# Optimization experiments

Measured on AMD Instinct MI355X. Metric: run time of the kernel, lower is better.

Reference implementation:

```python
import jax, jax.numpy as jnp
import numpy as np

G, N_PER_G, V, H, DIN, DOUT, E = 1024, 64, 32, 128, 128, 10, 1048576
N = G * N_PER_G


def _lin(key, fan_in, fan_out):
    k1, k2 = jax.random.split(key)
    s = 1.0 / np.sqrt(fan_in)
    return (jax.random.uniform(k1, (fan_in, fan_out), jnp.float32, -s, s),
            jax.random.uniform(k2, (fan_out,), jnp.float32, -s, s))


def setup_inputs() -> dict:
    key = jax.random.key(0)
    ks = jax.random.split(key, 16)
    x = jax.random.normal(ks[0], (N, DIN), jnp.float32)
    # random edges constrained within each graph's contiguous node block
    gid = jax.random.randint(ks[1], (E,), 0, G)
    src = gid * N_PER_G + jax.random.randint(ks[2], (E,), 0, N_PER_G)
    dst = gid * N_PER_G + jax.random.randint(ks[3], (E,), 0, N_PER_G)
    edge_index = jnp.stack([src, dst]).astype(jnp.int64)
    batch = jnp.repeat(jnp.arange(G, dtype=jnp.int64), N_PER_G)
    edge_weights = jnp.ones((G, N_PER_G, V), jnp.float32) / V  # uniform init
    vemb = jax.random.normal(ks[4], (G, V, H), jnp.float32)
    vemb = vemb / jnp.linalg.norm(vemb, axis=-1, keepdims=True)
    W_emb, b_emb = _lin(ks[5], DIN, H)
    W_gcn, b_gcn = _lin(ks[6], H, H)
    aff_W1, aff_b1 = _lin(ks[7], H, H)
    aff_W2, aff_b2 = _lin(ks[8], H, H)
    vn_W1, vn_b1 = _lin(ks[9], H, H)
    vn_W2, vn_b2 = _lin(ks[10], H, H)
    mlp_W1, mlp_b1 = _lin(ks[11], H, H)
    mlp_W2, mlp_b2 = _lin(ks[12], H, DOUT)
    return dict(x=x, edge_index=edge_index, batch=batch, edge_weights=edge_weights,
                vemb=vemb, W_emb=W_emb, b_emb=b_emb, W_gcn=W_gcn, b_gcn=b_gcn,
                aff_W1=aff_W1, aff_b1=aff_b1, aff_W2=aff_W2, aff_b2=aff_b2,
                vn_W1=vn_W1, vn_b1=vn_b1, vn_W2=vn_W2, vn_b2=vn_b2,
                mlp_W1=mlp_W1, mlp_b1=mlp_b1, mlp_W2=mlp_W2, mlp_b2=mlp_b2)


def reference(x, edge_index, batch, edge_weights, vemb, W_emb, b_emb, W_gcn, b_gcn,
              aff_W1, aff_b1, aff_W2, aff_b2, vn_W1, vn_b1, vn_W2, vn_b2,
              mlp_W1, mlp_b1, mlp_W2, mlp_b2):
    n_nodes = x.shape[0]
    g, n, v = edge_weights.shape
    h = x @ W_emb + b_emb                                   # node embedding
    # GCNConv with self-loops and symmetric normalization
    hw = h @ W_gcn
    sl = jnp.arange(n_nodes)
    s = jnp.concatenate([edge_index[0], sl])
    d = jnp.concatenate([edge_index[1], sl])
    deg = jax.ops.segment_sum(jnp.ones_like(d, dtype=h.dtype), d, num_segments=n_nodes)
    inv = jax.lax.rsqrt(jnp.maximum(deg, 1.0))
    msg = hw[s] * (inv[s] * inv[d])[:, None]                # [E+N, H]
    h = jax.nn.relu(jax.ops.segment_sum(msg, d, num_segments=n_nodes) + b_gcn)
    # affinity MLP
    aff = jax.nn.relu(h @ aff_W1 + aff_b1) @ aff_W2 + aff_b2
    hg = h.reshape(g, n, -1)
    affg = aff.reshape(g, n, -1)
    # attention vs fixed normalized virtual-node embeddings
    att = jnp.einsum('gnh,gvh->gnv', affg, vemb) / jnp.sqrt(jnp.asarray(hg.shape[-1], h.dtype))
    ew = edge_weights * (1.0 + jax.nn.sigmoid(att))
    rs = ew.sum(axis=-1, keepdims=True)
    ew = ew / jnp.where(rs == 0, 1.0, rs)                   # row-normalize
    vn = jnp.einsum('gnv,gnh->gvh', ew, hg)                 # weighted scatter-pool
    vn = jax.nn.relu(vn @ vn_W1 + vn_b1) @ vn_W2 + vn_b2
    gf = vn.mean(axis=1)                                    # [G, H]
    return jax.nn.relu(gf @ mlp_W1 + mlp_b1) @ mlp_W2 + mlp_b2
```

## Files before the change

kernel.cpp:

```cpp
#include <hip/hip_runtime.h>
#include <hip/hip_bf16.h>
#include <cstddef>


#define EDGES 1048576
#define CAP 2048
#define SR 136
#define ST 72

typedef __attribute__((ext_vector_type(8))) short short8;
typedef __attribute__((ext_vector_type(4))) float f32x4;
typedef __hip_bfloat16 bf;
struct __align__(8) bf4 { bf v[4]; };

__global__ __launch_bounds__(256) void edge_hist(const int* __restrict__ ei,
                                                 unsigned* __restrict__ H)
{
    __shared__ unsigned lh[1024];
    int tid = threadIdx.x, b = blockIdx.x;
    for (int t = tid; t < 1024; t += 256) lh[t] = 0;
    __syncthreads();
    int base = b * 4096;
#pragma unroll 4
    for (int t = 0; t < 16; ++t) {
        int s = ei[base + t * 256 + tid];
        atomicAdd(&lh[s >> 6], 1u);
    }
    __syncthreads();
    for (int t = tid; t < 1024; t += 256) H[b * 1024 + t] = lh[t];
}

__global__ __launch_bounds__(256) void scan_conv(
    unsigned* __restrict__ H, unsigned* __restrict__ Tot,
    const float* __restrict__ w0, const float* __restrict__ w1,
    const float* __restrict__ w2, const float* __restrict__ w3,
    const float* __restrict__ w4, const float* __restrict__ w5,
    bf* __restrict__ outw)
{
    int b = blockIdx.x;
    if (b < 256) {
        int wv = threadIdx.x >> 6, lane = threadIdx.x & 63;
        int g = b * 4 + wv;
        unsigned v[4];
#pragma unroll
        for (int c = 0; c < 4; ++c) v[c] = H[(c * 64 + lane) * 1024 + g];
        unsigned run = 0;
#pragma unroll
        for (int c = 0; c < 4; ++c) {
            unsigned s = v[c];
            unsigned incl = s;
#pragma unroll
            for (int d = 1; d < 64; d <<= 1) {
                unsigned t = __shfl_up(incl, d);
                if (lane >= d) incl += t;
            }
            H[(c * 64 + lane) * 1024 + g] = run + (incl - s);
            run += __shfl(incl, 63);
        }
        if (lane == 0) Tot[g] = run;
    } else {
        int idx = (b - 256) * 256 + threadIdx.x;
        int n = idx >> 7, k = idx & 127;
        int off = (((n >> 4) * 4 + (k >> 5)) * 512) + (n & 15) * 32 + (k & 31);
        const float* srcs[6] = { w0, w1, w2, w3, w4, w5 };
#pragma unroll
        for (int m = 0; m < 6; ++m) {
            float vv = (m == 3) ? srcs[m][n * 128 + k] : srcs[m][k * 128 + n];
            outw[m * 16384 + off] = __float2bfloat16(vv);
        }
    }
}

__global__ __launch_bounds__(256) void edge_scatter(const int* __restrict__ ei,
                                                    const unsigned* __restrict__ H,
                                                    unsigned short* __restrict__ sorted)
{
    __shared__ unsigned lh[1024];
    __shared__ unsigned hrow[1024];
    int tid = threadIdx.x, b = blockIdx.x;
    for (int t = tid; t < 1024; t += 256) { lh[t] = 0; hrow[t] = H[b * 1024 + t]; }
    __syncthreads();
    int base = b * 4096;
    for (int t = 0; t < 16; ++t) {
        int e = base + t * 256 + tid;
        int s = ei[e], d = ei[EDGES + e];
        int g = s >> 6;
        unsigned r = atomicAdd(&lh[g], 1u);
        unsigned o = hrow[g] + r;
        if (o < (unsigned)CAP)
            sorted[(unsigned)g * CAP + o] = (unsigned short)(((d & 63) << 6) | (s & 63));
    }
}

__device__ __forceinline__ void loadB(const bf* __restrict__ gW, int wv, int l15,
                                      int kofs, short8* B)
{
#pragma unroll
    for (int ks = 0; ks < 4; ++ks)
        B[ks] = *(const short8*)(gW + (wv * 4 + ks) * 512 + l15 * 32 + kofs);
}

template<int MT, int KS, int SA>
__device__ __forceinline__ void mmaAB(const bf* sA, int rowA, int l15, int kofs,
                                      const short8* B, f32x4* acc)
{
#pragma unroll
    for (int ks = 0; ks < KS; ++ks) {
        short8 a[MT];
#pragma unroll
        for (int m = 0; m < MT; ++m)
            a[m] = *(const short8*)(sA + (rowA + m * 16 + l15) * SA + ks * 32 + kofs);
#pragma unroll
        for (int m = 0; m < MT; ++m)
            acc[m] = __builtin_amdgcn_mfma_f32_16x16x32_bf16(a[m], B[ks], acc[m], 0, 0, 0);
    }
}

template<int NT, int KS, int SB>
__device__ __forceinline__ void mmaBA(const bf* sB, int rowB, int l15, int kofs,
                                      const short8* A, f32x4* acc)
{
#pragma unroll
    for (int ks = 0; ks < KS; ++ks) {
        short8 b[NT];
#pragma unroll
        for (int nt = 0; nt < NT; ++nt)
            b[nt] = *(const short8*)(sB + (rowB + nt * 16 + l15) * SB + ks * 32 + kofs);
#pragma unroll
        for (int nt = 0; nt < NT; ++nt)
            acc[nt] = __builtin_amdgcn_mfma_f32_16x16x32_bf16(A[ks], b[nt], acc[nt], 0, 0, 0);
    }
}

template<int MT, int KS, int SA, int SB>
__device__ __forceinline__ void mmaABlds(const bf* sA, int rowA, const bf* sB, int rowB,
                                         int l15, int kofs, f32x4* acc)
{
#pragma unroll
    for (int ks = 0; ks < KS; ++ks) {
        short8 bb = *(const short8*)(sB + (rowB + l15) * SB + ks * 32 + kofs);
        short8 a[MT];
#pragma unroll
        for (int m = 0; m < MT; ++m)
            a[m] = *(const short8*)(sA + (rowA + m * 16 + l15) * SA + ks * 32 + kofs);
#pragma unroll
        for (int m = 0; m < MT; ++m)
            acc[m] = __builtin_amdgcn_mfma_f32_16x16x32_bf16(a[m], bb, acc[m], 0, 0, 0);
    }
}

__global__ __launch_bounds__(512, 2) void fused_graph(
    const float* __restrict__ x, const float* __restrict__ edge_w,
    const float* __restrict__ vemb, const bf* __restrict__ gWb,
    const float* __restrict__ b_emb,  const float* __restrict__ b_gcn,
    const float* __restrict__ aff_b1, const float* __restrict__ aff_b2,
    const float* __restrict__ vn_b1,  const float* __restrict__ vn_b2,
    const float* __restrict__ mlp_W1, const float* __restrict__ mlp_b1,
    const float* __restrict__ mlp_W2, const float* __restrict__ mlp_b2,
    const unsigned short* __restrict__ sorted,
    const unsigned* __restrict__ Tot,
    float* __restrict__ out)
{
    __shared__ __align__(16) bf sRM1[64 * SR];
    __shared__ __align__(16) bf sRM2[64 * SR];
    __shared__ __align__(16) bf sT1 [128 * ST];
    __shared__ __align__(16) bf sT2 [128 * ST];
    __shared__ __align__(16) bf sAdj[64 * ST];
    __shared__ float sInv[64];
    __shared__ float sBatt[32];

    unsigned* cnt = (unsigned*)sT1;
    bf* sVemb = sAdj;
    float* sPart = (float*)(sAdj + 4352);
    bf* sS    = sT1;
    bf* sEwnT = sT1 + 4608;
    float* sT2f = (float*)sT2;

    const int tid = threadIdx.x;
    const int g = blockIdx.x;
    const int wv = tid >> 6;
    const int lane = tid & 63;
    const int l15 = lane & 15;
    const int q = lane >> 4;
    const int kofs = q * 8;
    const int c = wv * 16 + l15;
    const int fq = wv * 16 + q * 4;

    short8 Bp[4], Bn[4];
    loadB(gWb, wv, l15, kofs, Bp);
    loadB(gWb + 16384, wv, l15, kofs, Bn);
    float4 xreg[4];
    const float4* gx = (const float4*)(x + (size_t)g * 8192);
#pragma unroll
    for (int t = 0; t < 4; ++t) xreg[t] = gx[tid + t * 512];
    float4 vreg[2];
    const float4* gv = (const float4*)(vemb + (size_t)g * 4096);
#pragma unroll
    for (int t = 0; t < 2; ++t) vreg[t] = gv[tid + t * 512];
    const int p6row = (wv & 3) * 16;
    const int p6v   = (wv >> 2) * 16 + l15;
    float ewreg[4];
#pragma unroll
    for (int r = 0; r < 4; ++r)
        ewreg[r] = edge_w[(size_t)g * 2048 + (p6row + q * 4 + r) * 32 + p6v];
    float bias_g = b_gcn[c];
    unsigned ecnt = min(Tot[g], (unsigned)CAP);
    unsigned ebase = (unsigned)g * CAP;

#pragma unroll
    for (int t = 0; t < 2; ++t) cnt[tid * 2 + t] = 0u;
    __syncthreads();
    for (unsigned i = tid; i < ecnt; i += 512) {
        unsigned w = sorted[ebase + i];
        unsigned d = w >> 6, s = w & 63u;
        atomicAdd(&cnt[d * 16 + (s >> 2)], 1u << ((s & 3u) * 8));
    }
#pragma unroll
    for (int t = 0; t < 4; ++t) {
        int i = tid + t * 512;
        int row = i >> 5, c4 = i & 31;
        float4 w = xreg[t];
        bf4 tt;
        tt.v[0] = __float2bfloat16(w.x); tt.v[1] = __float2bfloat16(w.y);
        tt.v[2] = __float2bfloat16(w.z); tt.v[3] = __float2bfloat16(w.w);
        *(bf4*)(sRM1 + row * SR + c4 * 4) = tt;
    }
    __syncthreads();

    {
        int r = tid >> 3, q8 = tid & 7;
        float rs = 0.f;
#pragma unroll
        for (int t = 0; t < 2; ++t) {
            unsigned wd = cnt[r * 16 + q8 * 2 + t];
#pragma unroll
            for (int j = 0; j < 4; ++j) {
                int s = (q8 * 2 + t) * 4 + j;
                float v = (float)((wd >> (j * 8)) & 255u) + (s == r ? 1.f : 0.f);
                rs += v;
                sAdj[r * ST + s] = __float2bfloat16(v);
            }
        }
        rs += __shfl_xor(rs, 1);
        rs += __shfl_xor(rs, 2);
        rs += __shfl_xor(rs, 4);
        if (q8 == 0) sInv[r] = rsqrtf(rs);
    }
    {
        f32x4 acc[4] = {};
        mmaBA<4, 4, SR>(sRM1, 0, l15, kofs, Bp, acc);
        loadB(gWb + 2 * 16384, wv, l15, kofs, Bp);
        f32x4 b4 = *(const f32x4*)(b_emb + fq);
#pragma unroll
        for (int nt = 0; nt < 4; ++nt) {
            bf4 tv;
#pragma unroll
            for (int r = 0; r < 4; ++r) tv.v[r] = __float2bfloat16(acc[nt][r] + b4[r]);
            *(bf4*)(sRM2 + (nt * 16 + l15) * SR + fq) = tv;
        }
    }
    __syncthreads();

    {
        f32x4 acc[4] = {};
        mmaAB<4, 4, SR>(sRM2, 0, l15, kofs, Bn, acc);
        loadB(gWb + 3 * 16384, wv, l15, kofs, Bn);
#pragma unroll
        for (int m = 0; m < 4; ++m) {
            bf4 tv;
#pragma unroll
            for (int r = 0; r < 4; ++r)
                tv.v[r] = __float2bfloat16(acc[m][r] * sInv[m * 16 + q * 4 + r]);
            *(bf4*)(sT1 + c * ST + m * 16 + q * 4) = tv;
        }
    }
    __syncthreads();

    {
        f32x4 acc[4] = {};
        mmaABlds<4, 2, ST, ST>(sAdj, 0, sT1, wv * 16, l15, kofs, acc);
#pragma unroll
        for (int m = 0; m < 4; ++m) {
            bf4 tv;
#pragma unroll
            for (int r = 0; r < 4; ++r) {
                float v = fmaxf(acc[m][r] * sInv[m * 16 + q * 4 + r] + bias_g, 0.f);
                sRM1[(m * 16 + q * 4 + r) * SR + c] = __float2bfloat16(v);
                tv.v[r] = __float2bfloat16(v);
            }
            *(bf4*)(sT2 + c * ST + m * 16 + q * 4) = tv;
        }
    }
    __syncthreads();

    {
#pragma unroll
        for (int t = 0; t < 2; ++t) {
            int i = tid + t * 512;
            int v = i >> 5, o4 = i & 31;
            float4 w = vreg[t];
            bf4 tt;
            tt.v[0] = __float2bfloat16(w.x); tt.v[1] = __float2bfloat16(w.y);
            tt.v[2] = __float2bfloat16(w.z); tt.v[3] = __float2bfloat16(w.w);
            *(bf4*)(sVemb + v * SR + o4 * 4) = tt;
        }
        f32x4 acc[4] = {};
        mmaBA<4, 4, SR>(sRM1, 0, l15, kofs, Bp, acc);
        loadB(gWb + 4 * 16384, wv, l15, kofs, Bp);
        f32x4 b4 = *(const f32x4*)(aff_b1 + fq);
#pragma unroll
        for (int nt = 0; nt < 4; ++nt) {
            bf4 tv;
#pragma unroll
            for (int r = 0; r < 4; ++r)
                tv.v[r] = __float2bfloat16(fmaxf(acc[nt][r] + b4[r], 0.f));
            *(bf4*)(sRM2 + (nt * 16 + l15) * SR + fq) = tv;
        }
    }
    __syncthreads();

    {
        f32x4 acc[2] = {};
        mmaBA<2, 4, SR>(sVemb, 0, l15, kofs, Bn, acc);
        loadB(gWb + 5 * 16384, wv, l15, kofs, Bn);
#pragma unroll
        for (int nt = 0; nt < 2; ++nt) {
            bf4 tv;
#pragma unroll
            for (int r = 0; r < 4; ++r) tv.v[r] = __float2bfloat16(acc[nt][r]);
            *(bf4*)(sS + (nt * 16 + l15) * SR + fq) = tv;
        }
        if (tid < 256) {
            int v = tid >> 3, sg = tid & 7;
            float s = 0.f;
            const bf* pv = sVemb + v * SR + sg * 16;
            const float* pb = aff_b2 + sg * 16;
#pragma unroll
            for (int o = 0; o < 16; ++o) s += pb[o] * __bfloat162float(pv[o]);
            s += __shfl_xor(s, 1); s += __shfl_xor(s, 2); s += __shfl_xor(s, 4);
            if (sg == 0) sBatt[v] = s;
        }
    }
    __syncthreads();

    {
        f32x4 acc = {};
        const int hv = wv >> 2;
#pragma unroll
        for (int ks = 0; ks < 4; ++ks) {
            short8 bb = *(const short8*)(sS + (hv * 16 + l15) * SR + ks * 32 + kofs);
            short8 a  = *(const short8*)(sRM2 + (p6row + l15) * SR + ks * 32 + kofs);
            acc = __builtin_amdgcn_mfma_f32_16x16x32_bf16(a, bb, acc, 0, 0, 0);
        }
        const float sc = 0.08838834764831845f;
        float bt = sBatt[p6v];
        float e[4];
#pragma unroll
        for (int r = 0; r < 4; ++r) {
            float att = (acc[r] + bt) * sc;
            e[r] = ewreg[r] * (1.f + 1.f / (1.f + __expf(-att)));
            float rs = e[r];
            rs += __shfl_xor(rs, 1); rs += __shfl_xor(rs, 2);
            rs += __shfl_xor(rs, 4); rs += __shfl_xor(rs, 8);
            if (l15 == 0) sPart[hv * 64 + p6row + q * 4 + r] = rs;
        }
        __syncthreads();
        bf4 tv;
#pragma unroll
        for (int r = 0; r < 4; ++r) {
            float rs = sPart[p6row + q * 4 + r] + sPart[64 + p6row + q * 4 + r];
            tv.v[r] = __float2bfloat16(e[r] / rs);
        }
        *(bf4*)(sEwnT + (hv * 16 + l15) * ST + p6row + q * 4) = tv;
    }
    __syncthreads();

    {
        f32x4 acc[2] = {};
#pragma unroll
        for (int ks = 0; ks < 2; ++ks) {
            short8 af = *(const short8*)(sT2 + (wv * 16 + l15) * ST + ks * 32 + kofs);
            short8 b0 = *(const short8*)(sEwnT + l15 * ST + ks * 32 + kofs);
            short8 b1 = *(const short8*)(sEwnT + (16 + l15) * ST + ks * 32 + kofs);
            acc[0] = __builtin_amdgcn_mfma_f32_16x16x32_bf16(af, b0, acc[0], 0, 0, 0);
            acc[1] = __builtin_amdgcn_mfma_f32_16x16x32_bf16(af, b1, acc[1], 0, 0, 0);
        }
#pragma unroll
        for (int nt = 0; nt < 2; ++nt) {
            bf4 tv;
#pragma unroll
            for (int r = 0; r < 4; ++r) tv.v[r] = __float2bfloat16(acc[nt][r]);
            *(bf4*)(sRM1 + (nt * 16 + l15) * SR + fq) = tv;
        }
    }
    __syncthreads();

    {
        f32x4 acc[2] = {};
        mmaBA<2, 4, SR>(sRM1, 0, l15, kofs, Bp, acc);
        f32x4 b4 = *(const f32x4*)(vn_b1 + fq);
#pragma unroll
        for (int nt = 0; nt < 2; ++nt) {
            bf4 tv;
#pragma unroll
            for (int r = 0; r < 4; ++r)
                tv.v[r] = __float2bfloat16(fmaxf(acc[nt][r] + b4[r], 0.f));
            *(bf4*)(sRM1 + (32 + nt * 16 + l15) * SR + fq) = tv;
        }
    }
    __syncthreads();

    {
        float bias_v2 = vn_b2[c];
        f32x4 acc[2] = {};
        mmaAB<2, 4, SR>(sRM1 + 32 * SR, 0, l15, kofs, Bn, acc);
#pragma unroll
        for (int m = 0; m < 2; ++m)
#pragma unroll
            for (int r = 0; r < 4; ++r)
                sT2f[c * 34 + m * 16 + q * 4 + r] = acc[m][r] + bias_v2;
    }
    __syncthreads();

    float* sF = (float*)sRM2;
    if (tid < 128) {
        float s = 0.f;
#pragma unroll
        for (int v = 0; v < 32; ++v) s += sT2f[tid * 34 + v];
        sF[tid] = s * 0.03125f;
    }
    __syncthreads();

    {
        int o = tid & 127, hh = tid >> 7;
        const float* w = mlp_W1 + (size_t)(hh * 32) * 128 + o;
        float a = 0.f;
#pragma unroll 8
        for (int k = 0; k < 32; ++k) a = fmaf(sF[hh * 32 + k], w[k * 128], a);
        sF[128 + hh * 128 + o] = a;
    }
    __syncthreads();
    if (tid < 128)
        sF[640 + tid] = fmaxf(sF[128 + tid] + sF[256 + tid] + sF[384 + tid]
                              + sF[512 + tid] + mlp_b1[tid], 0.f);
    __syncthreads();

    if (tid < 80) {
        int oo = tid >> 3, jg = tid & 7;
        float p = 0.f;
#pragma unroll
        for (int t2 = 0; t2 < 16; ++t2) {
            int j = jg * 16 + t2;
            p = fmaf(sF[640 + j], mlp_W2[j * 10 + oo], p);
        }
        p += __shfl_xor(p, 1); p += __shfl_xor(p, 2); p += __shfl_xor(p, 4);
        if (jg == 0) out[g * 10 + oo] = p + mlp_b2[oo];
    }
}

extern "C" void kernel_launch(void* const* d_in, const int* in_sizes, int n_in,
                              void* d_out, int out_size, void* d_ws, size_t ws_size,
                              hipStream_t stream)
{
    const float* x       = (const float*)d_in[0];
    const int*   ei      = (const int*)  d_in[1];
    const float* edge_w  = (const float*)d_in[3];
    const float* vemb    = (const float*)d_in[4];
    const float* W_emb   = (const float*)d_in[5];
    const float* b_emb   = (const float*)d_in[6];
    const float* W_gcn   = (const float*)d_in[7];
    const float* b_gcn   = (const float*)d_in[8];
    const float* aff_W1  = (const float*)d_in[9];
    const float* aff_b1  = (const float*)d_in[10];
    const float* aff_W2  = (const float*)d_in[11];
    const float* aff_b2  = (const float*)d_in[12];
    const float* vn_W1   = (const float*)d_in[13];
    const float* vn_b1   = (const float*)d_in[14];
    const float* vn_W2   = (const float*)d_in[15];
    const float* vn_b2   = (const float*)d_in[16];
    const float* mlp_W1  = (const float*)d_in[17];
    const float* mlp_b1  = (const float*)d_in[18];
    const float* mlp_W2  = (const float*)d_in[19];
    const float* mlp_b2  = (const float*)d_in[20];

    char* ws = (char*)d_ws;
    unsigned short* sorted = (unsigned short*)ws;
    unsigned* H    = (unsigned*)(ws + (4u << 20));
    unsigned* Tot  = (unsigned*)(ws + (5u << 20));
    bf*       gWb  = (bf*)      (ws + (5u << 20) + 65536);

    edge_hist  <<<dim3(256), dim3(256), 0, stream>>>(ei, H);
    scan_conv  <<<dim3(320), dim3(256), 0, stream>>>(
        H, Tot, W_emb, W_gcn, aff_W1, aff_W2, vn_W1, vn_W2, gWb);
    edge_scatter<<<dim3(256),dim3(256), 0, stream>>>(ei, H, sorted);
    fused_graph<<<dim3(1024), dim3(512), 0, stream>>>(
        x, edge_w, vemb, gWb, b_emb, b_gcn, aff_b1, aff_b2,
        vn_b1, vn_b2, mlp_W1, mlp_b1, mlp_W2, mlp_b2,
        sorted, Tot, (float*)d_out);
}
```

Baseline: 181.9 us.

## Process two graphs per block to amortize weight fragment loads and barriers

Each block now handles two graphs instead of one, so the grid is halved. Shared buffers are doubled, and every stage loops over both graphs before a shared barrier. The intent is to reuse each register-resident weight B fragment across two graphs, halving global weight-fragment loads and barriers per graph. The cost is double the LDS and more registers per block, and launch bounds drop to one block per SM, which reduces occupancy and latency hiding.

```diff
diff --git a/kernel.cpp b/kernel.cpp
--- a/kernel.cpp
+++ b/kernel.cpp
@@ -149,7 +149,7 @@
     }
 }
 
-__global__ __launch_bounds__(512, 2) void fused_graph(
+__global__ __launch_bounds__(512, 1) void fused_graph(
     const float* __restrict__ x, const float* __restrict__ edge_w,
     const float* __restrict__ vemb, const bf* __restrict__ gWb,
     const float* __restrict__ b_emb,  const float* __restrict__ b_gcn,
@@ -161,23 +161,16 @@
     const unsigned* __restrict__ Tot,
     float* __restrict__ out)
 {
-    __shared__ __align__(16) bf sRM1[64 * SR];
-    __shared__ __align__(16) bf sRM2[64 * SR];
-    __shared__ __align__(16) bf sT1 [128 * ST];
-    __shared__ __align__(16) bf sT2 [128 * ST];
-    __shared__ __align__(16) bf sAdj[64 * ST];
-    __shared__ float sInv[64];
-    __shared__ float sBatt[32];
-
-    unsigned* cnt = (unsigned*)sT1;
-    bf* sVemb = sAdj;
-    float* sPart = (float*)(sAdj + 4352);
-    bf* sS    = sT1;
-    bf* sEwnT = sT1 + 4608;
-    float* sT2f = (float*)sT2;
+    __shared__ __align__(16) bf sRM1[2 * 64 * SR];
+    __shared__ __align__(16) bf sRM2[2 * 64 * SR];
+    __shared__ __align__(16) bf sT1 [2 * 128 * ST];
+    __shared__ __align__(16) bf sT2 [2 * 128 * ST];
+    __shared__ __align__(16) bf sAdj[2 * 64 * ST];
+    __shared__ float sInv[2 * 64];
+    __shared__ float sBatt[2 * 32];
 
     const int tid = threadIdx.x;
-    const int g = blockIdx.x;
+    const int g0 = blockIdx.x * 2;
     const int wv = tid >> 6;
     const int lane = tid & 63;
     const int l15 = lane & 15;
@@ -185,128 +178,164 @@
     const int kofs = q * 8;
     const int c = wv * 16 + l15;
     const int fq = wv * 16 + q * 4;
+    const int p6row = (wv & 3) * 16;
+    const int hv = wv >> 2;
+    const int p6v = hv * 16 + l15;
 
     short8 Bp[4], Bn[4];
     loadB(gWb, wv, l15, kofs, Bp);
     loadB(gWb + 16384, wv, l15, kofs, Bn);
-    float4 xreg[4];
-    const float4* gx = (const float4*)(x + (size_t)g * 8192);
-#pragma unroll
-    for (int t = 0; t < 4; ++t) xreg[t] = gx[tid + t * 512];
-    float4 vreg[2];
-    const float4* gv = (const float4*)(vemb + (size_t)g * 4096);
-#pragma unroll
-    for (int t = 0; t < 2; ++t) vreg[t] = gv[tid + t * 512];
-    const int p6row = (wv & 3) * 16;
-    const int p6v   = (wv >> 2) * 16 + l15;
-    float ewreg[4];
-#pragma unroll
-    for (int r = 0; r < 4; ++r)
-        ewreg[r] = edge_w[(size_t)g * 2048 + (p6row + q * 4 + r) * 32 + p6v];
+    float4 xreg[2][4];
+    float4 vreg[2][2];
+    float ewreg[2][4];
+    unsigned ecnt[2], ebase[2];
+#pragma unroll
+    for (int gg = 0; gg < 2; ++gg) {
+        const float4* gx = (const float4*)(x + (size_t)(g0 + gg) * 8192);
+#pragma unroll
+        for (int t = 0; t < 4; ++t) xreg[gg][t] = gx[tid + t * 512];
+        const float4* gv = (const float4*)(vemb + (size_t)(g0 + gg) * 4096);
+#pragma unroll
+        for (int t = 0; t < 2; ++t) vreg[gg][t] = gv[tid + t * 512];
+#pragma unroll
+        for (int r = 0; r < 4; ++r)
+            ewreg[gg][r] = edge_w[(size_t)(g0 + gg) * 2048
+                                  + (p6row + q * 4 + r) * 32 + p6v];
+        ecnt[gg] = min(Tot[g0 + gg], (unsigned)CAP);
+        ebase[gg] = (unsigned)(g0 + gg) * CAP;
+    }
     float bias_g = b_gcn[c];
-    unsigned ecnt = min(Tot[g], (unsigned)CAP);
-    unsigned ebase = (unsigned)g * CAP;
-
-#pragma unroll
-    for (int t = 0; t < 2; ++t) cnt[tid * 2 + t] = 0u;
-    __syncthreads();
-    for (unsigned i = tid; i < ecnt; i += 512) {
-        unsigned w = sorted[ebase + i];
-        unsigned d = w >> 6, s = w & 63u;
-        atomicAdd(&cnt[d * 16 + (s >> 2)], 1u << ((s & 3u) * 8));
-    }
-#pragma unroll
-    for (int t = 0; t < 4; ++t) {
-        int i = tid + t * 512;
-        int row = i >> 5, c4 = i & 31;
-        float4 w = xreg[t];
-        bf4 tt;
-        tt.v[0] = __float2bfloat16(w.x); tt.v[1] = __float2bfloat16(w.y);
-        tt.v[2] = __float2bfloat16(w.z); tt.v[3] = __float2bfloat16(w.w);
-        *(bf4*)(sRM1 + row * SR + c4 * 4) = tt;
-    }
-    __syncthreads();
-
-    {
-        int r = tid >> 3, q8 = tid & 7;
-        float rs = 0.f;
-#pragma unroll
-        for (int t = 0; t < 2; ++t) {
-            unsigned wd = cnt[r * 16 + q8 * 2 + t];
-#pragma unroll
-            for (int j = 0; j < 4; ++j) {
-                int s = (q8 * 2 + t) * 4 + j;
-                float v = (float)((wd >> (j * 8)) & 255u) + (s == r ? 1.f : 0.f);
-                rs += v;
-                sAdj[r * ST + s] = __float2bfloat16(v);
+
+#pragma unroll
+    for (int gg = 0; gg < 2; ++gg) {
+        unsigned* cntg = (unsigned*)(sT1 + gg * 128 * ST);
+#pragma unroll
+        for (int t = 0; t < 2; ++t) cntg[tid * 2 + t] = 0u;
+    }
+    __syncthreads();
+#pragma unroll
+    for (int gg = 0; gg < 2; ++gg) {
+        unsigned* cntg = (unsigned*)(sT1 + gg * 128 * ST);
+        bf* RM1g = sRM1 + gg * 64 * SR;
+        for (unsigned i = tid; i < ecnt[gg]; i += 512) {
+            unsigned w = sorted[ebase[gg] + i];
+            unsigned d = w >> 6, s = w & 63u;
+            atomicAdd(&cntg[d * 16 + (s >> 2)], 1u << ((s & 3u) * 8));
+        }
+#pragma unroll
+        for (int t = 0; t < 4; ++t) {
+            int i = tid + t * 512;
+            int row = i >> 5, c4 = i & 31;
+            float4 w = xreg[gg][t];
+            bf4 tt;
+            tt.v[0] = __float2bfloat16(w.x); tt.v[1] = __float2bfloat16(w.y);
+            tt.v[2] = __float2bfloat16(w.z); tt.v[3] = __float2bfloat16(w.w);
+            *(bf4*)(RM1g + row * SR + c4 * 4) = tt;
+        }
+    }
+    __syncthreads();
+
+#pragma unroll
+    for (int gg = 0; gg < 2; ++gg) {
+        unsigned* cntg = (unsigned*)(sT1 + gg * 128 * ST);
+        bf* Adjg = sAdj + gg * 64 * ST;
+        float* Invg = sInv + gg * 64;
+        {
+            int r = tid >> 3, q8 = tid & 7;
+            float rs = 0.f;
+#pragma unroll
+            for (int t = 0; t < 2; ++t) {
+                unsigned wd = cntg[r * 16 + q8 * 2 + t];
+#pragma unroll
+                for (int j = 0; j < 4; ++j) {
+                    int s = (q8 * 2 + t) * 4 + j;
+                    float v = (float)((wd >> (j * 8)) & 255u) + (s == r ? 1.f : 0.f);
+                    rs += v;
+                    Adjg[r * ST + s] = __float2bfloat16(v);
+                }
             }
-        }
-        rs += __shfl_xor(rs, 1);
-        rs += __shfl_xor(rs, 2);
-        rs += __shfl_xor(rs, 4);
-        if (q8 == 0) sInv[r] = rsqrtf(rs);
-    }
-    {
+            rs += __shfl_xor(rs, 1);
+            rs += __shfl_xor(rs, 2);
+            rs += __shfl_xor(rs, 4);
+            if (q8 == 0) Invg[r] = rsqrtf(rs);
+        }
+        bf* RM1g = sRM1 + gg * 64 * SR;
+        bf* RM2g = sRM2 + gg * 64 * SR;
+        {
+            f32x4 acc[4] = {};
+            mmaBA<4, 4, SR>(RM1g, 0, l15, kofs, Bp, acc);
+            f32x4 b4 = *(const f32x4*)(b_emb + fq);
+#pragma unroll
+            for (int nt = 0; nt < 4; ++nt) {
+                bf4 tv;
+#pragma unroll
+                for (int r = 0; r < 4; ++r) tv.v[r] = __float2bfloat16(acc[nt][r] + b4[r]);
+                *(bf4*)(RM2g + (nt * 16 + l15) * SR + fq) = tv;
+            }
+        }
+    }
+    loadB(gWb + 2 * 16384, wv, l15, kofs, Bp);
+    __syncthreads();
+
+#pragma unroll
+    for (int gg = 0; gg < 2; ++gg) {
+        bf* RM2g = sRM2 + gg * 64 * SR;
+        bf* T1g = sT1 + gg * 128 * ST;
+        float* Invg = sInv + gg * 64;
         f32x4 acc[4] = {};
-        mmaBA<4, 4, SR>(sRM1, 0, l15, kofs, Bp, acc);
-        loadB(gWb + 2 * 16384, wv, l15, kofs, Bp);
-        f32x4 b4 = *(const f32x4*)(b_emb + fq);
-#pragma unroll
-        for (int nt = 0; nt < 4; ++nt) {
-            bf4 tv;
-#pragma unroll
-            for (int r = 0; r < 4; ++r) tv.v[r] = __float2bfloat16(acc[nt][r] + b4[r]);
-            *(bf4*)(sRM2 + (nt * 16 + l15) * SR + fq) = tv;
-        }
-    }
-    __syncthreads();
-
-    {
-        f32x4 acc[4] = {};
-        mmaAB<4, 4, SR>(sRM2, 0, l15, kofs, Bn, acc);
-        loadB(gWb + 3 * 16384, wv, l15, kofs, Bn);
+        mmaAB<4, 4, SR>(RM2g, 0, l15, kofs, Bn, acc);
 #pragma unroll
         for (int m = 0; m < 4; ++m) {
             bf4 tv;
 #pragma unroll
             for (int r = 0; r < 4; ++r)
-                tv.v[r] = __float2bfloat16(acc[m][r] * sInv[m * 16 + q * 4 + r]);
-            *(bf4*)(sT1 + c * ST + m * 16 + q * 4) = tv;
-        }
-    }
-    __syncthreads();
-
-    {
+                tv.v[r] = __float2bfloat16(acc[m][r] * Invg[m * 16 + q * 4 + r]);
+            *(bf4*)(T1g + c * ST + m * 16 + q * 4) = tv;
+        }
+    }
+    loadB(gWb + 3 * 16384, wv, l15, kofs, Bn);
+    __syncthreads();
+
+#pragma unroll
+    for (int gg = 0; gg < 2; ++gg) {
+        bf* Adjg = sAdj + gg * 64 * ST;
+        bf* T1g = sT1 + gg * 128 * ST;
+        bf* RM1g = sRM1 + gg * 64 * SR;
+        bf* T2g = sT2 + gg * 128 * ST;
+        float* Invg = sInv + gg * 64;
         f32x4 acc[4] = {};
-        mmaABlds<4, 2, ST, ST>(sAdj, 0, sT1, wv * 16, l15, kofs, acc);
+        mmaABlds<4, 2, ST, ST>(Adjg, 0, T1g, wv * 16, l15, kofs, acc);
 #pragma unroll
         for (int m = 0; m < 4; ++m) {
             bf4 tv;
 #pragma unroll
             for (int r = 0; r < 4; ++r) {
-                float v = fmaxf(acc[m][r] * sInv[m * 16 + q * 4 + r] + bias_g, 0.f);
-                sRM1[(m * 16 + q * 4 + r) * SR + c] = __float2bfloat16(v);
+                float v = fmaxf(acc[m][r] * Invg[m * 16 + q * 4 + r] + bias_g, 0.f);
+                RM1g[(m * 16 + q * 4 + r) * SR + c] = __float2bfloat16(v);
                 tv.v[r] = __float2bfloat16(v);
             }
-            *(bf4*)(sT2 + c * ST + m * 16 + q * 4) = tv;
-        }
-    }
-    __syncthreads();
-
-    {
+            *(bf4*)(T2g + c * ST + m * 16 + q * 4) = tv;
+        }
+    }
+    __syncthreads();
+
+#pragma unroll
+    for (int gg = 0; gg < 2; ++gg) {
+        bf* Vembg = sAdj + gg * 64 * ST;
 #pragma unroll
         for (int t = 0; t < 2; ++t) {
             int i = tid + t * 512;
             int v = i >> 5, o4 = i & 31;
-            float4 w = vreg[t];
+            float4 w = vreg[gg][t];
             bf4 tt;
             tt.v[0] = __float2bfloat16(w.x); tt.v[1] = __float2bfloat16(w.y);
             tt.v[2] = __float2bfloat16(w.z); tt.v[3] = __float2bfloat16(w.w);
-            *(bf4*)(sVemb + v * SR + o4 * 4) = tt;
-        }
+            *(bf4*)(Vembg + v * SR + o4 * 4) = tt;
+        }
+        bf* RM1g = sRM1 + gg * 64 * SR;
+        bf* RM2g = sRM2 + gg * 64 * SR;
         f32x4 acc[4] = {};
-        mmaBA<4, 4, SR>(sRM1, 0, l15, kofs, Bp, acc);
-        loadB(gWb + 4 * 16384, wv, l15, kofs, Bp);
+        mmaBA<4, 4, SR>(RM1g, 0, l15, kofs, Bp, acc);
         f32x4 b4 = *(const f32x4*)(aff_b1 + fq);
 #pragma unroll
         for (int nt = 0; nt < 4; ++nt) {
@@ -314,74 +343,92 @@
 #pragma unroll
             for (int r = 0; r < 4; ++r)
                 tv.v[r] = __float2bfloat16(fmaxf(acc[nt][r] + b4[r], 0.f));
-            *(bf4*)(sRM2 + (nt * 16 + l15) * SR + fq) = tv;
-        }
-    }
-    __syncthreads();
-
-    {
+            *(bf4*)(RM2g + (nt * 16 + l15) * SR + fq) = tv;
+        }
+    }
+    loadB(gWb + 4 * 16384, wv, l15, kofs, Bp);
+    __syncthreads();
+
+#pragma unroll
+    for (int gg = 0; gg < 2; ++gg) {
+        bf* Vembg = sAdj + gg * 64 * ST;
+        bf* Sg = sT1 + gg * 128 * ST;
+        float* Battg = sBatt + gg * 32;
         f32x4 acc[2] = {};
-        mmaBA<2, 4, SR>(sVemb, 0, l15, kofs, Bn, acc);
-        loadB(gWb + 5 * 16384, wv, l15, kofs, Bn);
+        mmaBA<2, 4, SR>(Vembg, 0, l15, kofs, Bn, acc);
 #pragma unroll
         for (int nt = 0; nt < 2; ++nt) {
             bf4 tv;
 #pragma unroll
             for (int r = 0; r < 4; ++r) tv.v[r] = __float2bfloat16(acc[nt][r]);
-            *(bf4*)(sS + (nt * 16 + l15) * SR + fq) = tv;
+            *(bf4*)(Sg + (nt * 16 + l15) * SR + fq) = tv;
         }
         if (tid < 256) {
             int v = tid >> 3, sg = tid & 7;
             float s = 0.f;
-            const bf* pv = sVemb + v * SR + sg * 16;
+            const bf* pv = Vembg + v * SR + sg * 16;
             const float* pb = aff_b2 + sg * 16;
 #pragma unroll
             for (int o = 0; o < 16; ++o) s += pb[o] * __bfloat162float(pv[o]);
             s += __shfl_xor(s, 1); s += __shfl_xor(s, 2); s += __shfl_xor(s, 4);
-            if (sg == 0) sBatt[v] = s;
-        }
-    }
-    __syncthreads();
-
-    {
+            if (sg == 0) Battg[v] = s;
+        }
+    }
+    loadB(gWb + 5 * 16384, wv, l15, kofs, Bn);
+    __syncthreads();
+
+    float e2[2][4];
+#pragma unroll
+    for (int gg = 0; gg < 2; ++gg) {
+        bf* RM2g = sRM2 + gg * 64 * SR;
+        bf* Sg = sT1 + gg * 128 * ST;
+        float* Battg = sBatt + gg * 32;
+        float* Partg = (float*)(sAdj + gg * 64 * ST + 4352);
         f32x4 acc = {};
-        const int hv = wv >> 2;
 #pragma unroll
         for (int ks = 0; ks < 4; ++ks) {
-            short8 bb = *(const short8*)(sS + (hv * 16 + l15) * SR + ks * 32 + kofs);
-            short8 a  = *(const short8*)(sRM2 + (p6row + l15) * SR + ks * 32 + kofs);
+            short8 bb = *(const short8*)(Sg + (hv * 16 + l15) * SR + ks * 32 + kofs);
+            short8 a  = *(const short8*)(RM2g + (p6row + l15) * SR + ks * 32 + kofs);
             acc = __builtin_amdgcn_mfma_f32_16x16x32_bf16(a, bb, acc, 0, 0, 0);
         }
         const float sc = 0.08838834764831845f;
-        float bt = sBatt[p6v];
-        float e[4];
+        float bt = Battg[p6v];
 #pragma unroll
         for (int r = 0; r < 4; ++r) {
             float att = (acc[r] + bt) * sc;
-            e[r] = ewreg[r] * (1.f + 1.f / (1.f + __expf(-att)));
-            float rs = e[r];
+            e2[gg][r] = ewreg[gg][r] * (1.f + 1.f / (1.f + __expf(-att)));
+            float rs = e2[gg][r];
             rs += __shfl_xor(rs, 1); rs += __shfl_xor(rs, 2);
             rs += __shfl_xor(rs, 4); rs += __shfl_xor(rs, 8);
-            if (l15 == 0) sPart[hv * 64 + p6row + q * 4 + r] = rs;
-        }
-        __syncthreads();
+            if (l15 == 0) Partg[hv * 64 + p6row + q * 4 + r] = rs;
+        }
+    }
+    __syncthreads();
+#pragma unroll
+    for (int gg = 0; gg < 2; ++gg) {
+        float* Partg = (float*)(sAdj + gg * 64 * ST + 4352);
+        bf* EwnTg = sT1 + gg * 128 * ST + 4608;
         bf4 tv;
 #pragma unroll
         for (int r = 0; r < 4; ++r) {
-            float rs = sPart[p6row + q * 4 + r] + sPart[64 + p6row + q * 4 + r];
-            tv.v[r] = __float2bfloat16(e[r] / rs);
-        }
-        *(bf4*)(sEwnT + (hv * 16 + l15) * ST + p6row + q * 4) = tv;
-    }
-    __syncthreads();
-
-    {
+            float rs = Partg[p6row + q * 4 + r] + Partg[64 + p6row + q * 4 + r];
+            tv.v[r] = __float2bfloat16(e2[gg][r] / rs);
+        }
+        *(bf4*)(EwnTg + (hv * 16 + l15) * ST + p6row + q * 4) = tv;
+    }
+    __syncthreads();
+
+#pragma unroll
+    for (int gg = 0; gg < 2; ++gg) {
+        bf* T2g = sT2 + gg * 128 * ST;
+        bf* EwnTg = sT1 + gg * 128 * ST + 4608;
+        bf* RM1g = sRM1 + gg * 64 * SR;
         f32x4 acc[2] = {};
 #pragma unroll
         for (int ks = 0; ks < 2; ++ks) {
-            short8 af = *(const short8*)(sT2 + (wv * 16 + l15) * ST + ks * 32 + kofs);
-            short8 b0 = *(const short8*)(sEwnT + l15 * ST + ks * 32 + kofs);
-            short8 b1 = *(const short8*)(sEwnT + (16 + l15) * ST + ks * 32 + kofs);
+            short8 af = *(const short8*)(T2g + (wv * 16 + l15) * ST + ks * 32 + kofs);
+            short8 b0 = *(const short8*)(EwnTg + l15 * ST + ks * 32 + kofs);
+            short8 b1 = *(const short8*)(EwnTg + (16 + l15) * ST + ks * 32 + kofs);
             acc[0] = __builtin_amdgcn_mfma_f32_16x16x32_bf16(af, b0, acc[0], 0, 0, 0);
             acc[1] = __builtin_amdgcn_mfma_f32_16x16x32_bf16(af, b1, acc[1], 0, 0, 0);
         }
@@ -390,14 +437,16 @@
             bf4 tv;
 #pragma unroll
             for (int r = 0; r < 4; ++r) tv.v[r] = __float2bfloat16(acc[nt][r]);
-            *(bf4*)(sRM1 + (nt * 16 + l15) * SR + fq) = tv;
-        }
-    }
-    __syncthreads();
-
-    {
+            *(bf4*)(RM1g + (nt * 16 + l15) * SR + fq) = tv;
+        }
+    }
+    __syncthreads();
+
+#pragma unroll
+    for (int gg = 0; gg < 2; ++gg) {
+        bf* RM1g = sRM1 + gg * 64 * SR;
         f32x4 acc[2] = {};
-        mmaBA<2, 4, SR>(sRM1, 0, l15, kofs, Bp, acc);
+        mmaBA<2, 4, SR>(RM1g, 0, l15, kofs, Bp, acc);
         f32x4 b4 = *(const f32x4*)(vn_b1 + fq);
 #pragma unroll
         for (int nt = 0; nt < 2; ++nt) {
@@ -405,56 +454,75 @@
 #pragma unroll
             for (int r = 0; r < 4; ++r)
                 tv.v[r] = __float2bfloat16(fmaxf(acc[nt][r] + b4[r], 0.f));
-            *(bf4*)(sRM1 + (32 + nt * 16 + l15) * SR + fq) = tv;
+            *(bf4*)(RM1g + (32 + nt * 16 + l15) * SR + fq) = tv;
         }
     }
     __syncthreads();
 
     {
         float bias_v2 = vn_b2[c];
-        f32x4 acc[2] = {};
-        mmaAB<2, 4, SR>(sRM1 + 32 * SR, 0, l15, kofs, Bn, acc);
-#pragma unroll
-        for (int m = 0; m < 2; ++m)
-#pragma unroll
-            for (int r = 0; r < 4; ++r)
-                sT2f[c * 34 + m * 16 + q * 4 + r] = acc[m][r] + bias_v2;
-    }
-    __syncthreads();
-
-    float* sF = (float*)sRM2;
-    if (tid < 128) {
-        float s = 0.f;
-#pragma unroll
-        for (int v = 0; v < 32; ++v) s += sT2f[tid * 34 + v];
-        sF[tid] = s * 0.03125f;
-    }
-    __syncthreads();
-
-    {
+#pragma unroll
+        for (int gg = 0; gg < 2; ++gg) {
+            bf* RM1g = sRM1 + gg * 64 * SR;
+            float* T2fg = (float*)(sT2 + gg * 128 * ST);
+            f32x4 acc[2] = {};
+            mmaAB<2, 4, SR>(RM1g + 32 * SR, 0, l15, kofs, Bn, acc);
+#pragma unroll
+            for (int m = 0; m < 2; ++m)
+#pragma unroll
+                for (int r = 0; r < 4; ++r)
+                    T2fg[c * 34 + m * 16 + q * 4 + r] = acc[m][r] + bias_v2;
+        }
+    }
+    __syncthreads();
+
+#pragma unroll
+    for (int gg = 0; gg < 2; ++gg) {
+        float* T2fg = (float*)(sT2 + gg * 128 * ST);
+        float* sFg = (float*)(sRM2 + gg * 64 * SR);
+        if (tid < 128) {
+            float s = 0.f;
+#pragma unroll
+            for (int v = 0; v < 32; ++v) s += T2fg[tid * 34 + v];
+            sFg[tid] = s * 0.03125f;
+        }
+    }
+    __syncthreads();
+
+#pragma unroll
+    for (int gg = 0; gg < 2; ++gg) {
+        float* sFg = (float*)(sRM2 + gg * 64 * SR);
         int o = tid & 127, hh = tid >> 7;
         const float* w = mlp_W1 + (size_t)(hh * 32) * 128 + o;
         float a = 0.f;
 #pragma unroll 8
-        for (int k = 0; k < 32; ++k) a = fmaf(sF[hh * 32 + k], w[k * 128], a);
-        sF[128 + hh * 128 + o] = a;
-    }
-    __syncthreads();
-    if (tid < 128)
-        sF[640 + tid] = fmaxf(sF[128 + tid] + sF[256 + tid] + sF[384 + tid]
-                              + sF[512 + tid] + mlp_b1[tid], 0.f);
-    __syncthreads();
-
-    if (tid < 80) {
-        int oo = tid >> 3, jg = tid & 7;
-        float p = 0.f;
-#pragma unroll
-        for (int t2 = 0; t2 < 16; ++t2) {
-            int j = jg * 16 + t2;
-            p = fmaf(sF[640 + j], mlp_W2[j * 10 + oo], p);
-        }
-        p += __shfl_xor(p, 1); p += __shfl_xor(p, 2); p += __shfl_xor(p, 4);
-        if (jg == 0) out[g * 10 + oo] = p + mlp_b2[oo];
+        for (int k = 0; k < 32; ++k) a = fmaf(sFg[hh * 32 + k], w[k * 128], a);
+        sFg[128 + hh * 128 + o] = a;
+    }
+    __syncthreads();
+#pragma unroll
+    for (int gg = 0; gg < 2; ++gg) {
+        float* sFg = (float*)(sRM2 + gg * 64 * SR);
+        if (tid < 128)
+            sFg[640 + tid] = fmaxf(sFg[128 + tid] + sFg[256 + tid] + sFg[384 + tid]
+                                   + sFg[512 + tid] + mlp_b1[tid], 0.f);
+    }
+    __syncthreads();
+
+#pragma unroll
+    for (int gg = 0; gg < 2; ++gg) {
+        float* sFg = (float*)(sRM2 + gg * 64 * SR);
+        if (tid < 80) {
+            int oo = tid >> 3, jg = tid & 7;
+            float p = 0.f;
+#pragma unroll
+            for (int t2 = 0; t2 < 16; ++t2) {
+                int j = jg * 16 + t2;
+                p = fmaf(sFg[640 + j], mlp_W2[j * 10 + oo], p);
+            }
+            p += __shfl_xor(p, 1); p += __shfl_xor(p, 2); p += __shfl_xor(p, 4);
+            if (jg == 0) out[(g0 + gg) * 10 + oo] = p + mlp_b2[oo];
+        }
     }
 }
 
@@ -493,7 +561,7 @@
     scan_conv  <<<dim3(320), dim3(256), 0, stream>>>(
         H, Tot, W_emb, W_gcn, aff_W1, aff_W2, vn_W1, vn_W2, gWb);
     edge_scatter<<<dim3(256),dim3(256), 0, stream>>>(ei, H, sorted);
-    fused_graph<<<dim3(1024), dim3(512), 0, stream>>>(
+    fused_graph<<<dim3(512), dim3(512), 0, stream>>>(
         x, edge_w, vemb, gWb, b_emb, b_gcn, aff_b1, aff_b2,
         vn_b1, vn_b2, mlp_W1, mlp_b1, mlp_W2, mlp_b2,
         sorted, Tot, (float*)d_out);
```

Result: slower. 189.6 us (+4.2%).
